# Kernel optimization log

Measured on AMD Instinct MI355X. Metric: run time of the kernel, lower is better.

Reference implementation:

```python
import jax, jax.numpy as jnp
import numpy as np

B, S, P, E, H, FF = 4, 16, 256, 768, 12, 3072
HD = E // H
LN_EPS = 1e-5


def _layernorm(x, g, b):
    m = jnp.mean(x, axis=-1, keepdims=True)
    v = jnp.mean((x - m) ** 2, axis=-1, keepdims=True)
    return (x - m) * jax.lax.rsqrt(v + LN_EPS) * g + b


def _qkv(x, wqkv, bqkv):
    # wqkv: [3, E, E] (in, out layout), bqkv: [3, E]
    qkv = jnp.einsum('bspe,tef->tbspf', x, wqkv) + bqkv[:, None, None, None, :]
    q, k, v = qkv
    b, s, p, e = x.shape
    shp = (b, s, p, H, HD)
    return q.reshape(shp), k.reshape(shp), v.reshape(shp)


def spatial_attn(x, wqkv, bqkv, wo, bo, g, beta):
    q, k, v = _qkv(x, wqkv, bqkv)  # [b,s,p,n,d]
    scale = 1.0 / np.sqrt(HD).astype(np.float32)
    scores = jnp.einsum('bsind,bsjnd->bsnij', q, k) * scale  # [b,s,n,p,p]
    attn = jax.nn.softmax(scores, axis=-1)
    out = jnp.einsum('bsnij,bsjnd->bsind', attn, v)  # [b,s,p,n,d]
    out = out.reshape(x.shape)
    out = out @ wo + bo
    return _layernorm(x + out, g, beta)


def temporal_attn(x, wqkv, bqkv, wo, bo, g, beta):
    q, k, v = _qkv(x, wqkv, bqkv)  # [b,s,p,n,d]
    scale = 1.0 / np.sqrt(HD).astype(np.float32)
    scores = jnp.einsum('bipnd,bjpnd->bpnij', q, k) * scale  # [b,p,n,s,s]
    s = x.shape[1]
    causal = jnp.tril(jnp.ones((s, s), dtype=bool))
    scores = jnp.where(causal, scores, jnp.float32(-jnp.inf))
    attn = jax.nn.softmax(scores, axis=-1)
    out = jnp.einsum('bpnij,bjpnd->bipnd', attn, v)  # [b,s,p,n,d]
    out = out.reshape(x.shape)
    out = out @ wo + bo
    return _layernorm(x + out, g, beta)


def ffn(x, w1, b1, w2, b2, g, beta):
    h = jax.nn.relu(x @ w1 + b1)
    out = h @ w2 + b2
    return _layernorm(x + out, g, beta)


def setup_inputs() -> dict:
    key = jax.random.key(0)
    ks = jax.random.split(key, 16)
    w = lambda k, shp: (jax.random.normal(k, shp, dtype=jnp.float32) * 0.02)
    inp = {
        'x': jax.random.normal(ks[0], (B, S, P, E), dtype=jnp.float32),
        'sa_wqkv': w(ks[1], (3, E, E)), 'sa_bqkv': jnp.zeros((3, E), jnp.float32),
        'sa_wo': w(ks[2], (E, E)), 'sa_bo': jnp.zeros((E,), jnp.float32),
        'sa_g': jnp.ones((E,), jnp.float32), 'sa_b': jnp.zeros((E,), jnp.float32),
        'ta_wqkv': w(ks[3], (3, E, E)), 'ta_bqkv': jnp.zeros((3, E), jnp.float32),
        'ta_wo': w(ks[4], (E, E)), 'ta_bo': jnp.zeros((E,), jnp.float32),
        'ta_g': jnp.ones((E,), jnp.float32), 'ta_b': jnp.zeros((E,), jnp.float32),
        'f_w1': w(ks[5], (E, FF)), 'f_b1': jnp.zeros((FF,), jnp.float32),
        'f_w2': w(ks[6], (FF, E)), 'f_b2': jnp.zeros((E,), jnp.float32),
        'f_g': jnp.ones((E,), jnp.float32), 'f_b': jnp.zeros((E,), jnp.float32),
    }
    return inp


def reference(x, sa_wqkv, sa_bqkv, sa_wo, sa_bo, sa_g, sa_b,
              ta_wqkv, ta_bqkv, ta_wo, ta_bo, ta_g, ta_b,
              f_w1, f_b1, f_w2, f_b2, f_g, f_b):
    x = spatial_attn(x, sa_wqkv, sa_bqkv, sa_wo, sa_bo, sa_g, sa_b)
    x = temporal_attn(x, ta_wqkv, ta_bqkv, ta_wo, ta_bo, ta_g, ta_b)
    x = ffn(x, f_w1, f_b1, f_w2, f_b2, f_g, f_b)
    return x
```

## Files before the change

### kernel.cpp

```cpp
#include <hip/hip_runtime.h>
#include <hip/hip_bf16.h>
#include <math.h>

constexpr int Bc = 4, Sc = 16, Pc = 256, Ec = 768, Hc = 12, HDc = 64, FFc = 3072;
constexpr int Mrows = Bc * Sc * Pc;
constexpr size_t ME = (size_t)Mrows * Ec;

typedef __attribute__((ext_vector_type(4))) float f32x4;
typedef __attribute__((ext_vector_type(8))) short s16x8;
typedef __attribute__((ext_vector_type(4))) short s16x4;

__device__ __forceinline__ short f2bf(float f) {
  union { float f; unsigned u; } v; v.f = f;
  unsigned r = (v.u + 0x7FFFu + ((v.u >> 16) & 1u)) >> 16;
  return (short)r;
}
__device__ __forceinline__ float bf2f(short s) {
  union { unsigned u; float f; } v; v.u = ((unsigned)(unsigned short)s) << 16;
  return v.f;
}

__device__ __forceinline__ void async16(const void* g, void* l) {
  __builtin_amdgcn_global_load_lds(
      (const __attribute__((address_space(1))) unsigned int*)g,
      (__attribute__((address_space(3))) unsigned int*)l, 16, 0, 0);
}

__device__ __forceinline__ void wtrans_tile(const float* __restrict__ W,
                                            short* __restrict__ Wt,
                                            int K, int N, int n0, int k0, int t)
{
  const int n  = n0 + (t >> 2);
  const int kc = k0 + (t & 3) * 16;
  short buf[16];
#pragma unroll
  for (int i = 0; i < 16; ++i)
    buf[i] = f2bf(W[(size_t)(kc + i) * N + n]);
  *reinterpret_cast<s16x8*>(&Wt[(size_t)n * K + kc])     = *reinterpret_cast<s16x8*>(&buf[0]);
  *reinterpret_cast<s16x8*>(&Wt[(size_t)n * K + kc + 8]) = *reinterpret_cast<s16x8*>(&buf[8]);
}

__global__ __launch_bounds__(256)
void prep_kernel(const float* __restrict__ x, short* __restrict__ Xb,
                 const float* __restrict__ saqkv, short* __restrict__ wt_saqkv,
                 const float* __restrict__ sawo,  short* __restrict__ wt_sawo,
                 const float* __restrict__ taqkv, short* __restrict__ wt_taqkv,
                 const float* __restrict__ tawo,  short* __restrict__ wt_tawo,
                 const float* __restrict__ fw1,   short* __restrict__ wt_fw1,
                 const float* __restrict__ fw2,   short* __restrict__ wt_fw2)
{
  const int b = blockIdx.x;
  const int t = threadIdx.x;
  constexpr size_t EE = (size_t)Ec * Ec;

  if (b < 432) {
    const int z = b / 144, tl = b % 144;
    wtrans_tile(saqkv + (size_t)z * EE, wt_saqkv + (size_t)z * EE,
                Ec, Ec, (tl % 12) * 64, (tl / 12) * 64, t);
  } else if (b < 576) {
    const int tl = b - 432;
    wtrans_tile(sawo, wt_sawo, Ec, Ec, (tl % 12) * 64, (tl / 12) * 64, t);
  } else if (b < 1008) {
    const int z = (b - 576) / 144, tl = (b - 576) % 144;
    wtrans_tile(taqkv + (size_t)z * EE, wt_taqkv + (size_t)z * EE,
                Ec, Ec, (tl % 12) * 64, (tl / 12) * 64, t);
  } else if (b < 1152) {
    const int tl = b - 1008;
    wtrans_tile(tawo, wt_tawo, Ec, Ec, (tl % 12) * 64, (tl / 12) * 64, t);
  } else if (b < 1728) {
    const int tl = b - 1152;
    wtrans_tile(fw1, wt_fw1, Ec, FFc, (tl % 48) * 64, (tl / 48) * 64, t);
  } else if (b < 2304) {
    const int tl = b - 1728;
    wtrans_tile(fw2, wt_fw2, FFc, Ec, (tl % 12) * 64, (tl / 12) * 64, t);
  } else {
    const size_t i = (size_t)(b - 2304) * 256 + t;
    const float4* p = reinterpret_cast<const float4*>(x + i * 8);
    float4 a = p[0], bb = p[1];
    s16x8 o = { f2bf(a.x), f2bf(a.y), f2bf(a.z), f2bf(a.w),
                f2bf(bb.x), f2bf(bb.y), f2bf(bb.z), f2bf(bb.w) };
    *reinterpret_cast<s16x8*>(Xb + i * 8) = o;
  }
}

#define LDFRAG(base, row, kc) \
  (*reinterpret_cast<const s16x8*>((base) + (row) * 128 + ((((kc) ^ ((row) & 7)) << 4))))

#define PH_READS(Aslot, Bslot, q, LDB) \
  do { \
    if (LDB) { \
      _Pragma("unroll") \
      for (int nj = 0; nj < 4; ++nj) { \
        bfr[nj][0] = LDFRAG((Bslot), wc * 64 + nj * 16 + l16, g); \
        bfr[nj][1] = LDFRAG((Bslot), wc * 64 + nj * 16 + l16, 4 + g); \
      } \
    } \
    _Pragma("unroll") \
    for (int mi = 0; mi < BMT; ++mi) { \
      const int arow = wr * (BMT * 64) + ((q) * BMT + mi) * 16 + l16; \
      afr[mi][0] = LDFRAG((Aslot), arow, g); \
      afr[mi][1] = LDFRAG((Aslot), arow, 4 + g); \
    } \
  } while (0)

#define PH_SYNC_MMA(q) \
  do { \
    __builtin_amdgcn_sched_barrier(0); \
    __builtin_amdgcn_s_barrier(); \
    asm volatile("s_waitcnt lgkmcnt(0)" ::: "memory"); \
    __builtin_amdgcn_sched_barrier(0); \
    __builtin_amdgcn_s_setprio(1); \
    _Pragma("unroll") \
    for (int mi = 0; mi < BMT; ++mi) \
      _Pragma("unroll") \
      for (int nj = 0; nj < 4; ++nj) { \
        acc[(q) * BMT + mi][nj] = __builtin_amdgcn_mfma_f32_16x16x32_bf16( \
            afr[mi][0], bfr[nj][0], acc[(q) * BMT + mi][nj], 0, 0, 0); \
        acc[(q) * BMT + mi][nj] = __builtin_amdgcn_mfma_f32_16x16x32_bf16( \
            afr[mi][1], bfr[nj][1], acc[(q) * BMT + mi][nj], 0, 0, 0); \
      } \
    __builtin_amdgcn_s_setprio(0); \
  } while (0)

#define PH_END \
  do { __builtin_amdgcn_s_barrier(); __builtin_amdgcn_sched_barrier(0); } while (0)

#define PH_END_VM \
  do { \
    asm volatile("s_waitcnt vmcnt(4)" ::: "memory"); \
    __builtin_amdgcn_sched_barrier(0); \
    __builtin_amdgcn_s_barrier(); \
    __builtin_amdgcn_sched_barrier(0); \
  } while (0)

template<int OUT, int BMT>
__global__ __launch_bounds__(512, 2)
void gemm256_kernel(const short* __restrict__ A, const short* __restrict__ Wt,
                    const float* __restrict__ biasg, const void* __restrict__ resv,
                    void* __restrict__ Cg, short* __restrict__ vt,
                    int M, int N, int K)
{
  constexpr int ASZ = BMT * 16384;
  __shared__ char smem[2 * (ASZ + 32768)];
  const int z = blockIdx.z;
  const short* __restrict__ Wz = Wt + (size_t)z * (size_t)N * K;
  const float* __restrict__ bz = biasg + (size_t)z * N;

  const int nwg = gridDim.x;
  const int swz = ((int)blockIdx.x & 7) * (nwg >> 3) + ((int)blockIdx.x >> 3);
  const int NT = N >> 8;
  const int bm = (swz / NT) * (BMT * 128);
  const int bn = (swz % NT) << 8;

  const int tid  = threadIdx.x;
  const int lane = tid & 63;
  const int wid  = tid >> 6;
  const int wr   = wid >> 2;
  const int wc   = wid & 3;
  const int l16  = lane & 15;
  const int g    = lane >> 4;

  char* const As0 = smem;
  char* const Bs0 = smem + ASZ;
  char* const As1 = smem + ASZ + 32768;
  char* const Bs1 = smem + 2 * ASZ + 32768;

  const int srow = lane >> 3;
  const int scol = ((lane & 7) ^ srow) * 8;
  const int ldso = wid * 1024;

  auto stageG = [&](const short* __restrict__ G, int grow0, int k0, char* ldsHalf) {
    const size_t r0 = (size_t)(grow0 + wid * 8 + srow);
    async16(G + r0 * K + (k0 + scol), ldsHalf + ldso);
    async16(G + (r0 + 64) * K + (k0 + scol), ldsHalf + 8192 + ldso);
  };

  f32x4 acc[BMT * 4][4];
  s16x8 bfr[4][2];
  s16x8 afr[BMT][2];
#pragma unroll
  for (int mi = 0; mi < BMT * 4; ++mi)
#pragma unroll
    for (int nj = 0; nj < 4; ++nj) acc[mi][nj] = f32x4{0.f, 0.f, 0.f, 0.f};

  const int ntile = K >> 6;
  const int nit   = ntile >> 1;

  stageG(A, bm, 0, As0);
  if (BMT == 2) stageG(A, bm + 128, 0, As0 + 16384);
  stageG(Wz, bn,       0,  Bs0);
  stageG(Wz, bn + 128, 0,  Bs0 + 16384);
  stageG(Wz, bn,       64, Bs1);
  stageG(Wz, bn + 128, 64, Bs1 + 16384);
  asm volatile("s_waitcnt vmcnt(4)" ::: "memory");
  __builtin_amdgcn_sched_barrier(0);
  __builtin_amdgcn_s_barrier();

  for (int j = 0; j < nit; ++j) {
    const int t1k = (2 * j + 1) << 6;
    const int t2k = (2 * j + 2) << 6;
    const int t3k = (2 * j + 3) << 6;
    const bool s2 = (2 * j + 2) < ntile;
    const bool s3 = (2 * j + 3) < ntile;

    PH_READS(As0, Bs0, 0, true);
    stageG(A, bm, t1k, As1);
    PH_SYNC_MMA(0);
    PH_END;

    PH_READS(As0, Bs0, 1, false);
    if (BMT == 2) stageG(A, bm + 128, t1k, As1 + 16384);
    PH_SYNC_MMA(1);
    PH_END;

    PH_READS(As0, Bs0, 2, false);
    if (s2) stageG(Wz, bn, t2k, Bs0);
    PH_SYNC_MMA(2);
    PH_END;

    PH_READS(As0, Bs0, 3, false);
    if (s2) stageG(Wz, bn + 128, t2k, Bs0 + 16384);
    PH_SYNC_MMA(3);
    PH_END_VM;

    PH_READS(As1, Bs1, 0, true);
    if (s2) stageG(A, bm, t2k, As0);
    PH_SYNC_MMA(0);
    PH_END;

    PH_READS(As1, Bs1, 1, false);
    if (BMT == 2) { if (s2) stageG(A, bm + 128, t2k, As0 + 16384); }
    PH_SYNC_MMA(1);
    PH_END;

    PH_READS(As1, Bs1, 2, false);
    if (s3) stageG(Wz, bn, t3k, Bs1);
    PH_SYNC_MMA(2);
    PH_END;

    PH_READS(As1, Bs1, 3, false);
    if (s3) stageG(Wz, bn + 128, t3k, Bs1 + 16384);
    PH_SYNC_MMA(3);
    PH_END_VM;
  }

  const short* resb = (const short*)resv;
  short* Cb = (short*)Cg + (size_t)z * (size_t)M * N;

#pragma unroll
  for (int mi = 0; mi < BMT * 4; ++mi) {
    const int row0 = bm + wr * (BMT * 64) + mi * 16 + g * 4;
#pragma unroll
    for (int nj = 0; nj < 4; ++nj) {
      const int col = bn + wc * 64 + nj * 16 + l16;
      if (OUT == 4 && z == 2) {
        const int bs2 = row0 >> 8, p0 = row0 & 255;
        const int h2 = col >> 6,  d2 = col & 63;
        const float bias = bz[col];
        s16x4 v = { f2bf(acc[mi][nj][0] + bias), f2bf(acc[mi][nj][1] + bias),
                    f2bf(acc[mi][nj][2] + bias), f2bf(acc[mi][nj][3] + bias) };
        *reinterpret_cast<s16x4*>(
            &vt[(((size_t)bs2 * 12 + h2) * 64 + d2) * 256 + p0]) = v;
      } else {
        const float bias = bz[col];
#pragma unroll
        for (int r = 0; r < 4; ++r) {
          float v = acc[mi][nj][r] + bias;
          size_t idx = (size_t)(row0 + r) * N + col;
          if (OUT == 3) v += bf2f(resb[idx]);
          if (OUT == 1) v = fmaxf(v, 0.f);
          Cb[idx] = f2bf(v);
        }
      }
    }
  }
}

__global__ __launch_bounds__(256, 3)
void spatial_attn_kernel(const short* __restrict__ Qg, const short* __restrict__ Kg,
                         const short* __restrict__ Vt, short* __restrict__ Og)
{
  const int bs = blockIdx.x;
  const int h  = blockIdx.y;

  __shared__ short Pl[4 * 32 * 64];

  const int tid  = threadIdx.x;
  const int lane = tid & 63;
  const int wid  = tid >> 6;
  const int l16  = lane & 15;
  const int g    = lane >> 4;
  const int q0   = blockIdx.z * 128 + wid * 32;
  char* Pw = (char*)Pl + wid * 4096;

  const size_t rowbase = (size_t)(bs * 256) * 768 + h * 64;
  const size_t vbase   = ((size_t)bs * 12 + h) * 64 * 256;

  s16x8 qa[2][2];
#pragma unroll
  for (int m = 0; m < 2; ++m)
#pragma unroll
    for (int ks = 0; ks < 2; ++ks)
      qa[m][ks] = *reinterpret_cast<const s16x8*>(
          &Qg[rowbase + (size_t)(q0 + m * 16 + l16) * 768 + ks * 32 + g * 8]);

  float mrun[2][4], lrun[2][4];
  f32x4 oac[2][4];
#pragma unroll
  for (int m = 0; m < 2; ++m)
#pragma unroll
    for (int r = 0; r < 4; ++r) { mrun[m][r] = -INFINITY; lrun[m][r] = 0.f; }
#pragma unroll
  for (int m = 0; m < 2; ++m)
#pragma unroll
    for (int n = 0; n < 4; ++n) oac[m][n] = f32x4{0.f, 0.f, 0.f, 0.f};

#pragma unroll
  for (int t = 0; t < 4; ++t) {
    const int key0 = t * 64;
    f32x4 sc[2][4];
#pragma unroll
    for (int m = 0; m < 2; ++m)
#pragma unroll
      for (int n = 0; n < 4; ++n) sc[m][n] = f32x4{0.f, 0.f, 0.f, 0.f};
#pragma unroll
    for (int ks = 0; ks < 2; ++ks) {
      s16x8 kf[4];
#pragma unroll
      for (int n = 0; n < 4; ++n) {
        const int key = key0 + n * 16 + l16;
        kf[n] = *reinterpret_cast<const s16x8*>(
            &Kg[rowbase + (size_t)key * 768 + ks * 32 + g * 8]);
      }
#pragma unroll
      for (int m = 0; m < 2; ++m)
#pragma unroll
        for (int n = 0; n < 4; ++n)
          sc[m][n] = __builtin_amdgcn_mfma_f32_16x16x32_bf16(qa[m][ks], kf[n], sc[m][n], 0, 0, 0);
    }
#pragma unroll
    for (int m = 0; m < 2; ++m)
#pragma unroll
      for (int n = 0; n < 4; ++n)
#pragma unroll
        for (int r = 0; r < 4; ++r) sc[m][n][r] *= 0.125f;

#pragma unroll
    for (int m = 0; m < 2; ++m) {
#pragma unroll
      for (int r = 0; r < 4; ++r) {
        float mx = fmaxf(fmaxf(sc[m][0][r], sc[m][1][r]), fmaxf(sc[m][2][r], sc[m][3][r]));
#pragma unroll
        for (int mk = 1; mk < 16; mk <<= 1) mx = fmaxf(mx, __shfl_xor(mx, mk, 64));
        const float mnew = fmaxf(mrun[m][r], mx);
        const float corr = __expf(mrun[m][r] - mnew);
        mrun[m][r] = mnew;
        float rs = 0.f;
#pragma unroll
        for (int n = 0; n < 4; ++n) {
          float p = __expf(sc[m][n][r] - mnew);
          sc[m][n][r] = p;
          rs += p;
        }
#pragma unroll
        for (int mk = 1; mk < 16; mk <<= 1) rs += __shfl_xor(rs, mk, 64);
        lrun[m][r] = lrun[m][r] * corr + rs;
#pragma unroll
        for (int nd = 0; nd < 4; ++nd) oac[m][nd][r] *= corr;
      }
    }
#pragma unroll
    for (int m = 0; m < 2; ++m)
#pragma unroll
      for (int n = 0; n < 4; ++n)
#pragma unroll
        for (int r = 0; r < 4; ++r) {
          const int q = m * 16 + g * 4 + r;
          const int key = n * 16 + l16;
          const int byte = q * 128 + (((key >> 3) ^ (q & 7)) * 16) + (key & 7) * 2;
          *reinterpret_cast<short*>(Pw + byte) = f2bf(sc[m][n][r]);
        }
#pragma unroll
    for (int ks = 0; ks < 2; ++ks) {
      s16x8 pa[2], vf[4];
#pragma unroll
      for (int m = 0; m < 2; ++m) {
        const int q = m * 16 + l16;
        const int s = ks * 4 + g;
        pa[m] = *reinterpret_cast<const s16x8*>(Pw + q * 128 + ((s ^ (q & 7)) * 16));
      }
#pragma unroll
      for (int nd = 0; nd < 4; ++nd) {
        const int d = nd * 16 + l16;
        const int key = key0 + ks * 32 + g * 8;
        vf[nd] = *reinterpret_cast<const s16x8*>(&Vt[vbase + (size_t)d * 256 + key]);
      }
#pragma unroll
      for (int m = 0; m < 2; ++m)
#pragma unroll
        for (int nd = 0; nd < 4; ++nd)
          oac[m][nd] = __builtin_amdgcn_mfma_f32_16x16x32_bf16(pa[m], vf[nd], oac[m][nd], 0, 0, 0);
    }
  }

#pragma unroll
  for (int m = 0; m < 2; ++m)
#pragma unroll
    for (int r = 0; r < 4; ++r) {
      const float inv = 1.f / lrun[m][r];
#pragma unroll
      for (int nd = 0; nd < 4; ++nd) oac[m][nd][r] *= inv;
    }
#pragma unroll
  for (int m = 0; m < 2; ++m)
#pragma unroll
    for (int nd = 0; nd < 4; ++nd)
#pragma unroll
      for (int r = 0; r < 4; ++r) {
        const int q = m * 16 + g * 4 + r;
        const int d = nd * 16 + l16;
        const int byte = q * 128 + (((d >> 3) ^ (q & 7)) * 16) + (d & 7) * 2;
        *reinterpret_cast<short*>(Pw + byte) = f2bf(oac[m][nd][r]);
      }
#pragma unroll
  for (int it = 0; it < 4; ++it) {
    const int slot = it * 64 + lane;
    const int q = slot >> 3, sl = slot & 7;
    const int d0 = (sl ^ (q & 7)) * 8;
    s16x8 v = *reinterpret_cast<const s16x8*>(Pw + slot * 16);
    *reinterpret_cast<s16x8*>(
        &Og[rowbase + (size_t)(q0 + q) * 768 + d0]) = v;
  }
}

__global__ __launch_bounds__(192)
void temporal_attn_kernel(const short* __restrict__ Qg, const short* __restrict__ Kg,
                          const short* __restrict__ Vg, short* __restrict__ Og)
{
  const int bp = blockIdx.x;
  const int b = bp >> 8, p = bp & 255;

  __shared__ short Ks[16 * 768];
  __shared__ short Vs[16 * 768];

  const int tid = threadIdx.x;
  const size_t gbase = ((size_t)(b * 16) * 256 + p) * 768;
  constexpr int SROW = 256 * 768;

  {
    const int half = tid / 96;
    const int cc   = tid - half * 96;
    const int c    = cc & 7, hs = cc >> 3;
    const int ldso = (c * 12 + hs) * 8;
#pragma unroll
    for (int it = 0; it < 8; ++it) {
      const int s = it * 2 + half;
      const size_t ga = gbase + (size_t)s * SROW + cc * 8;
      *reinterpret_cast<s16x8*>(&Ks[s * 768 + ldso]) =
          *reinterpret_cast<const s16x8*>(&Kg[ga]);
      *reinterpret_cast<s16x8*>(&Vs[s * 768 + ldso]) =
          *reinterpret_cast<const s16x8*>(&Vg[ga]);
    }
  }
  __syncthreads();

  const int h = tid % 12, i = tid / 12;
  const float scale = 0.125f;
  const size_t qoff = gbase + (size_t)i * SROW + h * 64;

  float q[HDc];
#pragma unroll
  for (int c = 0; c < 8; ++c) {
    s16x8 v = *reinterpret_cast<const s16x8*>(&Qg[qoff + c * 8]);
#pragma unroll
    for (int e = 0; e < 8; ++e) q[c * 8 + e] = bf2f(v[e]) * scale;
  }

  float m = -INFINITY, l = 0.f;
  float o[HDc];
#pragma unroll
  for (int d = 0; d < HDc; ++d) o[d] = 0.f;

  for (int j = 0; j <= i; ++j) {
    const short* kr = &Ks[j * 768];
    float s = 0.f;
#pragma unroll
    for (int c = 0; c < 8; ++c) {
      s16x8 kv = *reinterpret_cast<const s16x8*>(kr + (c * 12 + h) * 8);
#pragma unroll
      for (int e = 0; e < 8; ++e) s += q[c * 8 + e] * bf2f(kv[e]);
    }
    float mn   = fmaxf(m, s);
    float corr = __expf(m - mn);
    float pw   = __expf(s - mn);
    l = l * corr + pw;
    const short* vr = &Vs[j * 768];
#pragma unroll
    for (int c = 0; c < 8; ++c) {
      s16x8 vv = *reinterpret_cast<const s16x8*>(vr + (c * 12 + h) * 8);
#pragma unroll
      for (int e = 0; e < 8; ++e)
        o[c * 8 + e] = fmaf(pw, bf2f(vv[e]), o[c * 8 + e] * corr);
    }
    m = mn;
  }
  const float inv = 1.f / l;
  short* op = &Og[qoff];
#pragma unroll
  for (int c = 0; c < 8; ++c) {
    s16x8 v;
#pragma unroll
    for (int e = 0; e < 8; ++e) v[e] = f2bf(o[c * 8 + e] * inv);
    *reinterpret_cast<s16x8*>(op + c * 8) = v;
  }
}

template<bool OUTBF>
__global__ __launch_bounds__(256)
void layernorm_kernel(const short* __restrict__ U, const float* __restrict__ g,
                      const float* __restrict__ be, void* __restrict__ outv)
{
  const int tid  = threadIdx.x;
  const int lane = tid & 63, w = tid >> 6;
  const size_t row = (size_t)blockIdx.x * 4 + w;
  const short* u = U + row * Ec;

  float x[12];
#pragma unroll
  for (int c = 0; c < 3; ++c) {
    s16x4 v = *reinterpret_cast<const s16x4*>(&u[c * 256 + lane * 4]);
    x[c*4+0] = bf2f(v[0]); x[c*4+1] = bf2f(v[1]);
    x[c*4+2] = bf2f(v[2]); x[c*4+3] = bf2f(v[3]);
  }
  float s = 0.f;
#pragma unroll
  for (int k = 0; k < 12; ++k) s += x[k];
#pragma unroll
  for (int off = 32; off > 0; off >>= 1) s += __shfl_xor(s, off, 64);
  const float mean = s * (1.f / 768.f);

  float vs = 0.f;
#pragma unroll
  for (int k = 0; k < 12; ++k) { float d = x[k] - mean; vs += d * d; }
#pragma unroll
  for (int off = 32; off > 0; off >>= 1) vs += __shfl_xor(vs, off, 64);
  const float rs = rsqrtf(vs * (1.f / 768.f) + 1e-5f);

#pragma unroll
  for (int c = 0; c < 3; ++c) {
    int idx = c * 256 + lane * 4;
    float4 gv = *reinterpret_cast<const float4*>(&g[idx]);
    float4 bv = *reinterpret_cast<const float4*>(&be[idx]);
    float r0 = (x[c*4+0] - mean) * rs * gv.x + bv.x;
    float r1 = (x[c*4+1] - mean) * rs * gv.y + bv.y;
    float r2 = (x[c*4+2] - mean) * rs * gv.z + bv.z;
    float r3 = (x[c*4+3] - mean) * rs * gv.w + bv.w;
    if (OUTBF) {
      short* op = (short*)outv + row * Ec + idx;
      s16x4 v = { f2bf(r0), f2bf(r1), f2bf(r2), f2bf(r3) };
      *reinterpret_cast<s16x4*>(op) = v;
    } else {
      float* op = (float*)outv + row * Ec + idx;
      *reinterpret_cast<float4*>(op) = make_float4(r0, r1, r2, r3);
    }
  }
}

extern "C" void kernel_launch(void* const* d_in, const int* in_sizes, int n_in,
                              void* d_out, int out_size, void* d_ws, size_t ws_size,
                              hipStream_t stream)
{
  const float* x       = (const float*)d_in[0];
  const float* sa_wqkv = (const float*)d_in[1];
  const float* sa_bqkv = (const float*)d_in[2];
  const float* sa_wo   = (const float*)d_in[3];
  const float* sa_bo   = (const float*)d_in[4];
  const float* sa_g    = (const float*)d_in[5];
  const float* sa_b    = (const float*)d_in[6];
  const float* ta_wqkv = (const float*)d_in[7];
  const float* ta_bqkv = (const float*)d_in[8];
  const float* ta_wo   = (const float*)d_in[9];
  const float* ta_bo   = (const float*)d_in[10];
  const float* ta_g    = (const float*)d_in[11];
  const float* ta_b    = (const float*)d_in[12];
  const float* f_w1    = (const float*)d_in[13];
  const float* f_b1    = (const float*)d_in[14];
  const float* f_w2    = (const float*)d_in[15];
  const float* f_b2    = (const float*)d_in[16];
  const float* f_g     = (const float*)d_in[17];
  const float* f_b     = (const float*)d_in[18];

  float* out = (float*)d_out;

  constexpr size_t EE = (size_t)Ec * Ec;
  constexpr size_t WTOT = 3*EE + EE + 3*EE + EE + 2*(size_t)Ec*FFc;
  const size_t need = 12 * ME + 2 * WTOT;
  if (ws_size < need) return;

  short* Xb  = (short*)d_ws;
  short* Qb  = Xb + ME;
  short* Kb  = Qb + ME;
  short* Vtb = Qb + 2 * ME;
  short* Hb  = Qb;
  short* U   = Xb + 5 * ME;
  short* Wtb = U + ME;

  short* wt_sa_qkv = Wtb;
  short* wt_sa_wo  = wt_sa_qkv + 3 * EE;
  short* wt_ta_qkv = wt_sa_wo  + EE;
  short* wt_ta_wo  = wt_ta_qkv + 3 * EE;
  short* wt_f_w1   = wt_ta_wo  + EE;
  short* wt_f_w2   = wt_f_w1   + (size_t)Ec * FFc;

  prep_kernel<<<8448, 256, 0, stream>>>(
      x, Xb, sa_wqkv, wt_sa_qkv, sa_wo, wt_sa_wo,
      ta_wqkv, wt_ta_qkv, ta_wo, wt_ta_wo, f_w1, wt_f_w1, f_w2, wt_f_w2);

  const dim3 gQKV((Mrows / 256) * (Ec / 256), 1, 3);
  const dim3 gSQ ((Mrows / 128) * (Ec / 256), 1, 1);
  const dim3 gFF1((Mrows / 256) * (FFc / 256), 1, 1);

  gemm256_kernel<4, 2><<<gQKV, 512, 0, stream>>>(Xb, wt_sa_qkv, sa_bqkv, nullptr, Qb, Vtb, Mrows, Ec, Ec);
  spatial_attn_kernel<<<dim3(Bc * Sc, Hc, 2), 256, 0, stream>>>(Qb, Kb, Vtb, Qb);
  gemm256_kernel<3, 1><<<gSQ, 512, 0, stream>>>(Qb, wt_sa_wo, sa_bo, Xb, U, nullptr, Mrows, Ec, Ec);
  layernorm_kernel<true><<<Mrows / 4, 256, 0, stream>>>(U, sa_g, sa_b, Xb);

  gemm256_kernel<0, 2><<<gQKV, 512, 0, stream>>>(Xb, wt_ta_qkv, ta_bqkv, nullptr, Qb, nullptr, Mrows, Ec, Ec);
  temporal_attn_kernel<<<Bc * Pc, 192, 0, stream>>>(Qb, Kb, Vtb, Qb);
  gemm256_kernel<3, 1><<<gSQ, 512, 0, stream>>>(Qb, wt_ta_wo, ta_bo, Xb, U, nullptr, Mrows, Ec, Ec);
  layernorm_kernel<true><<<Mrows / 4, 256, 0, stream>>>(U, ta_g, ta_b, Xb);

  gemm256_kernel<1, 2><<<gFF1, 512, 0, stream>>>(Xb, wt_f_w1, f_b1, nullptr, Hb, nullptr, Mrows, FFc, Ec);
  gemm256_kernel<3, 1><<<gSQ, 512, 0, stream>>>(Hb, wt_f_w2, f_b2, Xb, U, nullptr, Mrows, Ec, FFc);
  layernorm_kernel<false><<<Mrows / 4, 256, 0, stream>>>(U, f_g, f_b, out);
}
```

Measured before the change: 578.1 us.

## Fuse output projection with residual add and LayerNorm in attention blocks

Adds a gemmln kernel in which each block computes 64 full rows of the 768-wide output projection. It then applies bias and residual and does the LayerNorm in-register, using a cross-wave reduction through shared memory. This replaces the separate GEMM and LayerNorm launches after spatial and temporal attention, and with them the U intermediate round-trip. The generic GEMM loses its BMT template parameter and always uses 256x256 tiles, so the FFN down-projection runs with half as many blocks. Risks: the fused kernel uses a simple double-buffered K=32 loop with a full vmcnt wait every step, and the FW2 grid may underfill the GPU.

```diff
diff --git a/kernel.cpp b/kernel.cpp
--- a/kernel.cpp
+++ b/kernel.cpp
@@ -96,8 +96,8 @@
       } \
     } \
     _Pragma("unroll") \
-    for (int mi = 0; mi < BMT; ++mi) { \
-      const int arow = wr * (BMT * 64) + ((q) * BMT + mi) * 16 + l16; \
+    for (int mi = 0; mi < 2; ++mi) { \
+      const int arow = wr * 128 + ((q) * 2 + mi) * 16 + l16; \
       afr[mi][0] = LDFRAG((Aslot), arow, g); \
       afr[mi][1] = LDFRAG((Aslot), arow, 4 + g); \
     } \
@@ -111,13 +111,13 @@
     __builtin_amdgcn_sched_barrier(0); \
     __builtin_amdgcn_s_setprio(1); \
     _Pragma("unroll") \
-    for (int mi = 0; mi < BMT; ++mi) \
+    for (int mi = 0; mi < 2; ++mi) \
       _Pragma("unroll") \
       for (int nj = 0; nj < 4; ++nj) { \
-        acc[(q) * BMT + mi][nj] = __builtin_amdgcn_mfma_f32_16x16x32_bf16( \
-            afr[mi][0], bfr[nj][0], acc[(q) * BMT + mi][nj], 0, 0, 0); \
-        acc[(q) * BMT + mi][nj] = __builtin_amdgcn_mfma_f32_16x16x32_bf16( \
-            afr[mi][1], bfr[nj][1], acc[(q) * BMT + mi][nj], 0, 0, 0); \
+        acc[(q) * 2 + mi][nj] = __builtin_amdgcn_mfma_f32_16x16x32_bf16( \
+            afr[mi][0], bfr[nj][0], acc[(q) * 2 + mi][nj], 0, 0, 0); \
+        acc[(q) * 2 + mi][nj] = __builtin_amdgcn_mfma_f32_16x16x32_bf16( \
+            afr[mi][1], bfr[nj][1], acc[(q) * 2 + mi][nj], 0, 0, 0); \
       } \
     __builtin_amdgcn_s_setprio(0); \
   } while (0)
@@ -133,15 +133,14 @@
     __builtin_amdgcn_sched_barrier(0); \
   } while (0)
 
-template<int OUT, int BMT>
+template<int OUT>
 __global__ __launch_bounds__(512, 2)
 void gemm256_kernel(const short* __restrict__ A, const short* __restrict__ Wt,
                     const float* __restrict__ biasg, const void* __restrict__ resv,
                     void* __restrict__ Cg, short* __restrict__ vt,
                     int M, int N, int K)
 {
-  constexpr int ASZ = BMT * 16384;
-  __shared__ char smem[2 * (ASZ + 32768)];
+  __shared__ char smem[131072];
   const int z = blockIdx.z;
   const short* __restrict__ Wz = Wt + (size_t)z * (size_t)N * K;
   const float* __restrict__ bz = biasg + (size_t)z * N;
@@ -149,7 +148,7 @@
   const int nwg = gridDim.x;
   const int swz = ((int)blockIdx.x & 7) * (nwg >> 3) + ((int)blockIdx.x >> 3);
   const int NT = N >> 8;
-  const int bm = (swz / NT) * (BMT * 128);
+  const int bm = (swz / NT) << 8;
   const int bn = (swz % NT) << 8;
 
   const int tid  = threadIdx.x;
@@ -161,9 +160,9 @@
   const int g    = lane >> 4;
 
   char* const As0 = smem;
-  char* const Bs0 = smem + ASZ;
-  char* const As1 = smem + ASZ + 32768;
-  char* const Bs1 = smem + 2 * ASZ + 32768;
+  char* const Bs0 = smem + 32768;
+  char* const As1 = smem + 65536;
+  char* const Bs1 = smem + 98304;
 
   const int srow = lane >> 3;
   const int scol = ((lane & 7) ^ srow) * 8;
@@ -175,23 +174,23 @@
     async16(G + (r0 + 64) * K + (k0 + scol), ldsHalf + 8192 + ldso);
   };
 
-  f32x4 acc[BMT * 4][4];
+  f32x4 acc[8][4];
   s16x8 bfr[4][2];
-  s16x8 afr[BMT][2];
-#pragma unroll
-  for (int mi = 0; mi < BMT * 4; ++mi)
+  s16x8 afr[2][2];
+#pragma unroll
+  for (int mi = 0; mi < 8; ++mi)
 #pragma unroll
     for (int nj = 0; nj < 4; ++nj) acc[mi][nj] = f32x4{0.f, 0.f, 0.f, 0.f};
 
   const int ntile = K >> 6;
   const int nit   = ntile >> 1;
 
-  stageG(A, bm, 0, As0);
-  if (BMT == 2) stageG(A, bm + 128, 0, As0 + 16384);
-  stageG(Wz, bn,       0,  Bs0);
-  stageG(Wz, bn + 128, 0,  Bs0 + 16384);
-  stageG(Wz, bn,       64, Bs1);
-  stageG(Wz, bn + 128, 64, Bs1 + 16384);
+  stageG(A,  bm,        0,  As0);
+  stageG(A,  bm + 128,  0,  As0 + 16384);
+  stageG(Wz, bn,        0,  Bs0);
+  stageG(Wz, bn + 128,  0,  Bs0 + 16384);
+  stageG(Wz, bn,        64, Bs1);
+  stageG(Wz, bn + 128,  64, Bs1 + 16384);
   asm volatile("s_waitcnt vmcnt(4)" ::: "memory");
   __builtin_amdgcn_sched_barrier(0);
   __builtin_amdgcn_s_barrier();
@@ -209,7 +208,7 @@
     PH_END;
 
     PH_READS(As0, Bs0, 1, false);
-    if (BMT == 2) stageG(A, bm + 128, t1k, As1 + 16384);
+    stageG(A, bm + 128, t1k, As1 + 16384);
     PH_SYNC_MMA(1);
     PH_END;
 
@@ -229,7 +228,7 @@
     PH_END;
 
     PH_READS(As1, Bs1, 1, false);
-    if (BMT == 2) { if (s2) stageG(A, bm + 128, t2k, As0 + 16384); }
+    if (s2) stageG(A, bm + 128, t2k, As0 + 16384);
     PH_SYNC_MMA(1);
     PH_END;
 
@@ -248,8 +247,8 @@
   short* Cb = (short*)Cg + (size_t)z * (size_t)M * N;
 
 #pragma unroll
-  for (int mi = 0; mi < BMT * 4; ++mi) {
-    const int row0 = bm + wr * (BMT * 64) + mi * 16 + g * 4;
+  for (int mi = 0; mi < 8; ++mi) {
+    const int row0 = bm + wr * 128 + mi * 16 + g * 4;
 #pragma unroll
     for (int nj = 0; nj < 4; ++nj) {
       const int col = bn + wc * 64 + nj * 16 + l16;
@@ -271,6 +270,133 @@
           if (OUT == 1) v = fmaxf(v, 0.f);
           Cb[idx] = f2bf(v);
         }
+      }
+    }
+  }
+}
+
+__global__ __launch_bounds__(512, 1)
+void gemmln_kernel(const short* __restrict__ A, const short* __restrict__ Wt,
+                   const float* __restrict__ bias, const short* __restrict__ res,
+                   const float* __restrict__ gam, const float* __restrict__ bet,
+                   short* __restrict__ outb, int K)
+{
+  __shared__ char Ag[2][4096];
+  __shared__ char Bg[2][49152];
+  __shared__ float redS[64][8];
+  __shared__ float redQ[64][8];
+
+  const int bm   = blockIdx.x * 64;
+  const int tid  = threadIdx.x;
+  const int lane = tid & 63;
+  const int w    = tid >> 6;
+  const int l16  = lane & 15;
+  const int g    = lane >> 4;
+
+  auto stage = [&](int k0, int slot) {
+#pragma unroll
+    for (int i = 0; i < 6; ++i) {
+      const int c  = w * 6 + i;
+      const int gc = c / 12, u = c % 12;
+      async16(Wt + (size_t)(u * 64 + lane) * K + k0 + gc * 8,
+              &Bg[slot][gc * 12288 + u * 1024]);
+    }
+    if (w < 4)
+      async16(A + (size_t)(bm + lane) * K + k0 + w * 8, &Ag[slot][w * 1024]);
+  };
+
+  f32x4 acc[4][6];
+#pragma unroll
+  for (int mi = 0; mi < 4; ++mi)
+#pragma unroll
+    for (int nj = 0; nj < 6; ++nj) acc[mi][nj] = f32x4{0.f, 0.f, 0.f, 0.f};
+
+  stage(0, 0);
+  asm volatile("s_waitcnt vmcnt(0)" ::: "memory");
+  __builtin_amdgcn_sched_barrier(0);
+  __builtin_amdgcn_s_barrier();
+
+  const int nstep = K >> 5;
+  for (int t = 0; t < nstep; ++t) {
+    const int cur = t & 1;
+    if (t + 1 < nstep) stage((t + 1) << 5, cur ^ 1);
+
+    s16x8 afr[4], bfr[6];
+#pragma unroll
+    for (int mi = 0; mi < 4; ++mi)
+      afr[mi] = *reinterpret_cast<const s16x8*>(
+          &Ag[cur][(g << 10) + ((mi * 16 + l16) << 4)]);
+#pragma unroll
+    for (int nj = 0; nj < 6; ++nj)
+      bfr[nj] = *reinterpret_cast<const s16x8*>(
+          &Bg[cur][g * 12288 + ((w * 96 + nj * 16 + l16) << 4)]);
+
+    asm volatile("s_waitcnt lgkmcnt(0)" ::: "memory");
+    __builtin_amdgcn_sched_barrier(0);
+    __builtin_amdgcn_s_setprio(1);
+#pragma unroll
+    for (int mi = 0; mi < 4; ++mi)
+#pragma unroll
+      for (int nj = 0; nj < 6; ++nj)
+        acc[mi][nj] = __builtin_amdgcn_mfma_f32_16x16x32_bf16(
+            afr[mi], bfr[nj], acc[mi][nj], 0, 0, 0);
+    __builtin_amdgcn_s_setprio(0);
+    asm volatile("s_waitcnt vmcnt(0)" ::: "memory");
+    __builtin_amdgcn_sched_barrier(0);
+    __builtin_amdgcn_s_barrier();
+  }
+
+  float biasv[6], gv[6], bv[6];
+#pragma unroll
+  for (int nj = 0; nj < 6; ++nj) {
+    const int col = w * 96 + nj * 16 + l16;
+    biasv[nj] = bias[col]; gv[nj] = gam[col]; bv[nj] = bet[col];
+  }
+#pragma unroll
+  for (int mi = 0; mi < 4; ++mi) {
+#pragma unroll
+    for (int r = 0; r < 4; ++r) {
+      const int lrow = mi * 16 + g * 4 + r;
+      const size_t rowoff = (size_t)(bm + lrow) * 768;
+      float s = 0.f, q = 0.f;
+#pragma unroll
+      for (int nj = 0; nj < 6; ++nj) {
+        const int col = w * 96 + nj * 16 + l16;
+        float v = acc[mi][nj][r] + biasv[nj] + bf2f(res[rowoff + col]);
+        acc[mi][nj][r] = v;
+        s += v; q += v * v;
+      }
+#pragma unroll
+      for (int mk = 1; mk < 16; mk <<= 1) {
+        s += __shfl_xor(s, mk, 64);
+        q += __shfl_xor(q, mk, 64);
+      }
+      if (l16 == 0) { redS[lrow][w] = s; redQ[lrow][w] = q; }
+    }
+  }
+  __syncthreads();
+  if (w == 0) {
+    float s = 0.f, q = 0.f;
+#pragma unroll
+    for (int i = 0; i < 8; ++i) { s += redS[lane][i]; q += redQ[lane][i]; }
+    const float mean = s * (1.f / 768.f);
+    const float var  = q * (1.f / 768.f) - mean * mean;
+    redS[lane][0] = mean;
+    redQ[lane][0] = rsqrtf(var + 1e-5f);
+  }
+  __syncthreads();
+#pragma unroll
+  for (int mi = 0; mi < 4; ++mi) {
+#pragma unroll
+    for (int r = 0; r < 4; ++r) {
+      const int lrow = mi * 16 + g * 4 + r;
+      const float mean = redS[lrow][0], rstd = redQ[lrow][0];
+      const size_t rowoff = (size_t)(bm + lrow) * 768;
+#pragma unroll
+      for (int nj = 0; nj < 6; ++nj) {
+        const int col = w * 96 + nj * 16 + l16;
+        float o = (acc[mi][nj][r] - mean) * rstd * gv[nj] + bv[nj];
+        outb[rowoff + col] = f2bf(o);
       }
     }
   }
@@ -617,20 +743,18 @@
       ta_wqkv, wt_ta_qkv, ta_wo, wt_ta_wo, f_w1, wt_f_w1, f_w2, wt_f_w2);
 
   const dim3 gQKV((Mrows / 256) * (Ec / 256), 1, 3);
-  const dim3 gSQ ((Mrows / 128) * (Ec / 256), 1, 1);
+  const dim3 gFW2((Mrows / 256) * (Ec / 256), 1, 1);
   const dim3 gFF1((Mrows / 256) * (FFc / 256), 1, 1);
 
-  gemm256_kernel<4, 2><<<gQKV, 512, 0, stream>>>(Xb, wt_sa_qkv, sa_bqkv, nullptr, Qb, Vtb, Mrows, Ec, Ec);
+  gemm256_kernel<4><<<gQKV, 512, 0, stream>>>(Xb, wt_sa_qkv, sa_bqkv, nullptr, Qb, Vtb, Mrows, Ec, Ec);
   spatial_attn_kernel<<<dim3(Bc * Sc, Hc, 2), 256, 0, stream>>>(Qb, Kb, Vtb, Qb);
-  gemm256_kernel<3, 1><<<gSQ, 512, 0, stream>>>(Qb, wt_sa_wo, sa_bo, Xb, U, nullptr, Mrows, Ec, Ec);
-  layernorm_kernel<true><<<Mrows / 4, 256, 0, stream>>>(U, sa_g, sa_b, Xb);
-
-  gemm256_kernel<0, 2><<<gQKV, 512, 0, stream>>>(Xb, wt_ta_qkv, ta_bqkv, nullptr, Qb, nullptr, Mrows, Ec, Ec);
+  gemmln_kernel<<<Mrows / 64, 512, 0, stream>>>(Qb, wt_sa_wo, sa_bo, Xb, sa_g, sa_b, Xb, Ec);
+
+  gemm256_kernel<0><<<gQKV, 512, 0, stream>>>(Xb, wt_ta_qkv, ta_bqkv, nullptr, Qb, nullptr, Mrows, Ec, Ec);
   temporal_attn_kernel<<<Bc * Pc, 192, 0, stream>>>(Qb, Kb, Vtb, Qb);
-  gemm256_kernel<3, 1><<<gSQ, 512, 0, stream>>>(Qb, wt_ta_wo, ta_bo, Xb, U, nullptr, Mrows, Ec, Ec);
-  layernorm_kernel<true><<<Mrows / 4, 256, 0, stream>>>(U, ta_g, ta_b, Xb);
-
-  gemm256_kernel<1, 2><<<gFF1, 512, 0, stream>>>(Xb, wt_f_w1, f_b1, nullptr, Hb, nullptr, Mrows, FFc, Ec);
-  gemm256_kernel<3, 1><<<gSQ, 512, 0, stream>>>(Hb, wt_f_w2, f_b2, Xb, U, nullptr, Mrows, Ec, FFc);
+  gemmln_kernel<<<Mrows / 64, 512, 0, stream>>>(Qb, wt_ta_wo, ta_bo, Xb, ta_g, ta_b, Xb, Ec);
+
+  gemm256_kernel<1><<<gFF1, 512, 0, stream>>>(Xb, wt_f_w1, f_b1, nullptr, Hb, nullptr, Mrows, FFc, Ec);
+  gemm256_kernel<3><<<gFW2, 512, 0, stream>>>(Hb, wt_f_w2, f_b2, Xb, U, nullptr, Mrows, Ec, FFc);
   layernorm_kernel<false><<<Mrows / 4, 256, 0, stream>>>(U, f_g, f_b, out);
 }
```

Measured after the change: 622.6 us. +7.7%, slower.
